# Kernel tuning notes

Measured on AMD Instinct MI355X. Metric: run time of the kernel, lower is better.

The kernel has to match this reference:

```python
import jax, jax.numpy as jnp
import numpy as np

# pywt db8 reconstruction low-pass filter (rec_lo); other filters derived per pywt conventions
_REC_LO = np.array([
    0.05441584224308161, 0.3128715909144659, 0.6756307362980128,
    0.5853546836548691, -0.015829105256023893, -0.2840155429624281,
    0.00047248457399797254, 0.128747426620186, -0.01736930100202211,
    -0.04408825393106472, 0.013981027917015516, 0.008746094047015655,
    -0.00487035299301066, -0.0003917403729959771, 0.0006754494059985568,
    -0.00011747678400228192], dtype=np.float64)
_F = 16
_REC_HI = np.array([(-1.0) ** k * _REC_LO[_F - 1 - k] for k in range(_F)])  # qmf
_DEC_LO = _REC_LO[::-1].copy()
_DEC_HI = _REC_HI[::-1].copy()
# lax.conv does cross-correlation; np.convolve flips the filter, so pre-flip here
_DEC_K = np.ascontiguousarray(np.stack([_DEC_LO[::-1], _DEC_HI[::-1]])[:, None, :])  # [2,1,F]
_REC_K = np.ascontiguousarray(np.stack([_REC_LO[::-1], _REC_HI[::-1]])[None, :, :])  # [1,2,F]
_THRESHOLD_FACTOR = 1.0


def _dwt_last(x):
    # single-level DWT along last axis, pywt 'symmetric' boundary mode
    shp = x.shape
    xf = x.reshape(-1, 1, shp[-1])
    xe = jnp.pad(xf, ((0, 0), (0, 0), (_F - 1, _F - 1)), mode='symmetric')[:, :, 1:]
    y = jax.lax.conv_general_dilated(xe, jnp.asarray(_DEC_K, x.dtype), (2,), 'VALID',
                                     dimension_numbers=('NCW', 'OIW', 'NCW'))  # [M,2,n]
    n = y.shape[-1]  # n = floor((N + F - 1) / 2)
    return y[:, 0].reshape(shp[:-1] + (n,)), y[:, 1].reshape(shp[:-1] + (n,))


def _idwt_last(ca, cd, out_len):
    # single-level inverse DWT along last axis; out_len = 2*n - F + 2
    shp = ca.shape
    n = shp[-1]
    m = int(np.prod(shp[:-1]))
    u = jnp.zeros((m, 2, 2 * n), ca.dtype)
    u = u.at[:, 0, ::2].set(ca.reshape(m, n)).at[:, 1, ::2].set(cd.reshape(m, n))
    ue = jnp.pad(u, ((0, 0), (0, 0), (_F - 1, _F - 1)))
    y = jax.lax.conv_general_dilated(ue, jnp.asarray(_REC_K, ca.dtype), (1,), 'VALID',
                                     dimension_numbers=('NCW', 'OIW', 'NCW'))[:, 0]
    return y[:, _F - 2:_F - 2 + out_len].reshape(shp[:-1] + (out_len,))


def _forward(x):
    B, H, W, C = x.shape
    M = B * C
    xm = jnp.transpose(x, (0, 3, 1, 2)).reshape(M, H, W)
    # level-1 wavedec2: rows (W axis) then columns (H axis)
    lo, hi = _dwt_last(xm)                               # [M,H,nW]
    ll, lh = _dwt_last(jnp.swapaxes(lo, -1, -2))         # [M,nW,nH]
    hl, hh = _dwt_last(jnp.swapaxes(hi, -1, -2))         # [M,nW,nH]
    # universal threshold from median abs of all detail subbands, per sample/channel
    det = jnp.concatenate([lh.reshape(M, -1), hl.reshape(M, -1), hh.reshape(M, -1)], axis=-1)
    sigma = jnp.median(jnp.abs(det), axis=-1) / 0.6745
    t = (sigma * jnp.sqrt(2.0 * jnp.log(float(H * W))) * _THRESHOLD_FACTOR)[:, None, None]
    soft = lambda c: jnp.sign(c) * jnp.maximum(jnp.abs(c) - t, 0.0)
    lh, hl, hh = soft(lh), soft(hl), soft(hh)
    # waverec2: inverse along H then along W
    nH = ll.shape[-1]
    Hr = 2 * nH - _F + 2
    rl = jnp.swapaxes(_idwt_last(ll, lh, Hr), -1, -2)    # [M,Hr,nW]
    rh = jnp.swapaxes(_idwt_last(hl, hh, Hr), -1, -2)    # [M,Hr,nW]
    nW = rl.shape[-1]
    y = _idwt_last(rl, rh, 2 * nW - _F + 2)              # [M,Hr,Wr]
    y = y[:, :H, :W].reshape(B, C, H, W)
    return jnp.transpose(y, (0, 2, 3, 1)).astype(x.dtype)


def setup_inputs() -> dict:
    key = jax.random.key(0)
    x = jax.random.normal(key, (32, 512, 512, 3), dtype=jnp.float32)
    return {"x": x}


def reference(x):
    return _forward(x)
```

## Files before the change

kernel.cpp:

```cpp
#include <hip/hip_runtime.h>
#include <math.h>

#define B_   32
#define H_   512
#define W_   512
#define C_   3
#define M_   96
#define NW_  263
#define NH_  263
#define DETPER 69169
#define DETTOT 207507
#define DETSTRIDE 207508
#define NVEC 51876
#define KRANK  103753u

#define SXS 144
#define CR  12

__device__ __constant__ float RLO[16] = {
    0.05441584224308161f,  0.3128715909144659f,   0.6756307362980128f,
    0.5853546836548691f,  -0.015829105256023893f, -0.2840155429624281f,
    0.00047248457399797254f, 0.128747426620186f,  -0.01736930100202211f,
   -0.04408825393106472f,  0.013981027917015516f,  0.008746094047015655f,
   -0.00487035299301066f, -0.0003917403729959771f, 0.0006754494059985568f,
   -0.00011747678400228192f};
__device__ __constant__ float RHI[16] = {
   -0.00011747678400228192f, -0.0006754494059985568f, -0.0003917403729959771f,
    0.00487035299301066f,     0.008746094047015655f,  -0.013981027917015516f,
   -0.04408825393106472f,     0.01736930100202211f,    0.128747426620186f,
   -0.00047248457399797254f, -0.2840155429624281f,     0.015829105256023893f,
    0.5853546836548691f,     -0.6756307362980128f,     0.3128715909144659f,
   -0.05441584224308161f};

__device__ __forceinline__ int refl(int q, int N) {
    if (q < 0)  return -q - 1;
    if (q >= N) return 2 * N - 1 - q;
    return q;
}

__device__ __forceinline__ float softthr(float v, float thr) {
    float a = fabsf(v) - thr;
    return a > 0.f ? copysignf(a, v) : 0.f;
}

__global__ __launch_bounds__(256) void k_zero(unsigned* __restrict__ p, int n) {
    int i = blockIdx.x * 256 + threadIdx.x;
    if (i < n) p[i] = 0u;
}

__global__ __launch_bounds__(256) void k_fwd(const float* __restrict__ x,
                                             float* __restrict__ ll,
                                             float* __restrict__ det) {
    __shared__ float sX[CR * SXS];
    __shared__ float sLO[46 * 64], sHI[46 * 64];
    const int m   = blockIdx.x;
    const int jw0 = blockIdx.y * 64;
    const int jh0 = blockIdx.z * 16;
    const int b = m / 3, c = m - 3 * (m / 3);
    const int tid = threadIdx.x;
    const int prow0 = 2 * jh0 - 14, pcol0 = 2 * jw0 - 14;
    for (int r0 = 0; r0 < 46; r0 += CR) {
        const int nr = (46 - r0) < CR ? (46 - r0) : CR;
        for (int l = tid; l < nr * 142; l += 256) {
            int rr = l / 142, cl = l - rr * 142;
            int h = refl(prow0 + r0 + rr, H_);
            int w = refl(pcol0 + cl, W_);
            sX[rr * SXS + cl] = x[((size_t)(b * H_ + h) * W_ + w) * C_ + c];
        }
        __syncthreads();
        for (int l = tid; l < nr * 64; l += 256) {
            int rr = l >> 6, j = l & 63;
            const float* px = &sX[rr * SXS + 2 * j];
            float al = 0.f, ah = 0.f;
#pragma unroll
            for (int k = 0; k < 16; ++k) {
                al = fmaf(px[k], RLO[k], al);
                ah = fmaf(px[k], RHI[k], ah);
            }
            sLO[(r0 + rr) * 64 + j] = al;
            sHI[(r0 + rr) * 64 + j] = ah;
        }
        __syncthreads();
    }
    const int tx = tid & 63, tg = tid >> 6;
    const int jw = jw0 + tx;
    if (jw >= NW_) return;
    float vl[22], vh[22];
#pragma unroll
    for (int s = 0; s < 22; ++s) {
        int row = 8 * tg + s;
        vl[s] = sLO[row * 64 + tx];
        vh[s] = sHI[row * 64 + tx];
    }
    float* llp = ll + (size_t)m * DETPER;
    float* dp  = det + (size_t)m * DETSTRIDE;
#pragma unroll
    for (int d = 0; d < 4; ++d) {
        int jh = jh0 + 4 * tg + d;
        if (jh >= NH_) continue;
        float a0 = 0.f, a1 = 0.f, a2 = 0.f, a3 = 0.f;
#pragma unroll
        for (int k = 0; k < 16; ++k) {
            float fl = vl[2 * d + k], fh = vh[2 * d + k];
            a0 = fmaf(fl, RLO[k], a0);
            a1 = fmaf(fl, RHI[k], a1);
            a2 = fmaf(fh, RLO[k], a2);
            a3 = fmaf(fh, RHI[k], a3);
        }
        size_t o = (size_t)jh * NW_ + jw;
        llp[o] = a0;
        dp[o] = a1;
        dp[DETPER + o] = a2;
        dp[2 * DETPER + o] = a3;
    }
}

__global__ __launch_bounds__(256) void k_hist1(const float* __restrict__ det,
                                               unsigned* __restrict__ hist) {
    __shared__ unsigned h[2048];
    const int tid = threadIdx.x, m = blockIdx.x;
    for (int i = tid; i < 2048; i += 256) h[i] = 0u;
    __syncthreads();
    const float* dp = det + (size_t)m * DETSTRIDE;
    const float4* dp4 = (const float4*)dp;
    const int stride = gridDim.y * 256;
    for (int v = blockIdx.y * 256 + tid; v < NVEC; v += stride) {
        float4 f = dp4[v];
        atomicAdd(&h[__float_as_uint(fabsf(f.x)) >> 21], 1u);
        atomicAdd(&h[__float_as_uint(fabsf(f.y)) >> 21], 1u);
        atomicAdd(&h[__float_as_uint(fabsf(f.z)) >> 21], 1u);
        atomicAdd(&h[__float_as_uint(fabsf(f.w)) >> 21], 1u);
    }
    if (blockIdx.y == 0 && tid < DETTOT - 4 * NVEC) {
        unsigned u = __float_as_uint(fabsf(dp[4 * NVEC + tid]));
        atomicAdd(&h[u >> 21], 1u);
    }
    __syncthreads();
    for (int i = tid; i < 2048; i += 256)
        if (h[i]) atomicAdd(&hist[m * 2048 + i], h[i]);
}

__global__ __launch_bounds__(256) void k_hist2(const float* __restrict__ det,
                                               const int* __restrict__ selBin1,
                                               unsigned* __restrict__ hist) {
    __shared__ unsigned h[2048];
    const int tid = threadIdx.x, m = blockIdx.x;
    const unsigned target = (unsigned)selBin1[m];
    for (int i = tid; i < 2048; i += 256) h[i] = 0u;
    __syncthreads();
    const float* dp = det + (size_t)m * DETSTRIDE;
    const float4* dp4 = (const float4*)dp;
    const int stride = gridDim.y * 256;
    for (int v = blockIdx.y * 256 + tid; v < NVEC; v += stride) {
        float4 f = dp4[v];
        unsigned a = __float_as_uint(fabsf(f.x));
        unsigned b = __float_as_uint(fabsf(f.y));
        unsigned c = __float_as_uint(fabsf(f.z));
        unsigned d = __float_as_uint(fabsf(f.w));
        if ((a >> 21) == target) atomicAdd(&h[(a >> 10) & 0x7FFu], 1u);
        if ((b >> 21) == target) atomicAdd(&h[(b >> 10) & 0x7FFu], 1u);
        if ((c >> 21) == target) atomicAdd(&h[(c >> 10) & 0x7FFu], 1u);
        if ((d >> 21) == target) atomicAdd(&h[(d >> 10) & 0x7FFu], 1u);
    }
    if (blockIdx.y == 0 && tid < DETTOT - 4 * NVEC) {
        unsigned u = __float_as_uint(fabsf(dp[4 * NVEC + tid]));
        if ((u >> 21) == target) atomicAdd(&h[(u >> 10) & 0x7FFu], 1u);
    }
    __syncthreads();
    for (int i = tid; i < 2048; i += 256)
        if (h[i]) atomicAdd(&hist[m * 2048 + i], h[i]);
}

__global__ __launch_bounds__(256) void k_hist3(const float* __restrict__ det,
                                               const int* __restrict__ selBin1,
                                               const int* __restrict__ selBin2,
                                               unsigned* __restrict__ hist) {
    __shared__ unsigned h[1024];
    const int tid = threadIdx.x, m = blockIdx.x;
    const unsigned target = ((unsigned)selBin1[m] << 11) | (unsigned)selBin2[m];
    for (int i = tid; i < 1024; i += 256) h[i] = 0u;
    __syncthreads();
    const float* dp = det + (size_t)m * DETSTRIDE;
    const float4* dp4 = (const float4*)dp;
    const int stride = gridDim.y * 256;
    for (int v = blockIdx.y * 256 + tid; v < NVEC; v += stride) {
        float4 f = dp4[v];
        unsigned a = __float_as_uint(fabsf(f.x));
        unsigned b = __float_as_uint(fabsf(f.y));
        unsigned c = __float_as_uint(fabsf(f.z));
        unsigned d = __float_as_uint(fabsf(f.w));
        if ((a >> 10) == target) atomicAdd(&h[a & 0x3FFu], 1u);
        if ((b >> 10) == target) atomicAdd(&h[b & 0x3FFu], 1u);
        if ((c >> 10) == target) atomicAdd(&h[c & 0x3FFu], 1u);
        if ((d >> 10) == target) atomicAdd(&h[d & 0x3FFu], 1u);
    }
    if (blockIdx.y == 0 && tid < DETTOT - 4 * NVEC) {
        unsigned u = __float_as_uint(fabsf(dp[4 * NVEC + tid]));
        if ((u >> 10) == target) atomicAdd(&h[u & 0x3FFu], 1u);
    }
    __syncthreads();
    for (int i = tid; i < 1024; i += 256)
        if (h[i]) atomicAdd(&hist[m * 1024 + i], h[i]);
}

__device__ int histSelect(unsigned* hist, int nb, unsigned rank, unsigned* rem) {
    __shared__ unsigned ps[256];
    __shared__ int s_bin;
    __shared__ unsigned s_rem;
    const int tid = threadIdx.x;
    if (tid == 0) { s_bin = 0; s_rem = 0; }
    const int per = nb >> 8;
    unsigned s = 0;
    for (int i = 0; i < per; ++i) s += hist[tid * per + i];
    ps[tid] = s;
    __syncthreads();
    for (int off = 1; off < 256; off <<= 1) {
        unsigned v = ps[tid];
        unsigned add = (tid >= off) ? ps[tid - off] : 0u;
        __syncthreads();
        ps[tid] = v + add;
        __syncthreads();
    }
    unsigned incl = ps[tid], excl = incl - s;
    if (rank >= excl && rank < incl) {
        unsigned cum = excl;
        for (int i = 0; i < per; ++i) {
            unsigned c = hist[tid * per + i];
            if (cum + c > rank) { s_bin = tid * per + i; s_rem = rank - cum; break; }
            cum += c;
        }
    }
    __syncthreads();
    int rbin = s_bin;
    unsigned rr = s_rem;
    __syncthreads();
    *rem = rr;
    return rbin;
}

__global__ __launch_bounds__(256) void k_sel2048(const unsigned* __restrict__ hist,
                                                 const unsigned* __restrict__ rankIn,
                                                 int* __restrict__ selBin,
                                                 unsigned* __restrict__ rankOut) {
    __shared__ unsigned h[2048];
    const int m = blockIdx.x, tid = threadIdx.x;
    for (int i = tid; i < 2048; i += 256) h[i] = hist[m * 2048 + i];
    __syncthreads();
    unsigned rank = rankIn ? rankIn[m] : KRANK;
    unsigned rem;
    int bin = histSelect(h, 2048, rank, &rem);
    if (tid == 0) { selBin[m] = bin; rankOut[m] = rem; }
}

__global__ __launch_bounds__(256) void k_sel3(const unsigned* __restrict__ hist,
                                              const unsigned* __restrict__ rankIn,
                                              const int* __restrict__ selBin1,
                                              const int* __restrict__ selBin2,
                                              float* __restrict__ tval) {
    __shared__ unsigned h[1024];
    const int m = blockIdx.x, tid = threadIdx.x;
    for (int i = tid; i < 1024; i += 256) h[i] = hist[m * 1024 + i];
    __syncthreads();
    unsigned rem;
    int low = histSelect(h, 1024, rankIn[m], &rem);
    if (tid == 0) {
        unsigned bits = ((unsigned)selBin1[m] << 21) | ((unsigned)selBin2[m] << 10) | (unsigned)low;
        double med = (double)__uint_as_float(bits);
        tval[m] = (float)(med / 0.6745 * 4.995327667046959);
    }
}

__global__ __launch_bounds__(256) void k_inv(const float* __restrict__ ll,
                                             const float* __restrict__ det,
                                             const float* __restrict__ tval,
                                             float* __restrict__ out) {
    __shared__ float sLL[23 * 40], sLH[23 * 40], sHL[23 * 40], sHH[23 * 40];
    __shared__ float sRL[32 * 40], sRH[32 * 40];
    const int m  = blockIdx.x;
    const int w0 = blockIdx.y * 64;
    const int t0 = blockIdx.z * 32;
    const int b = m / 3, c = m - 3 * (m / 3);
    const int tid = threadIdx.x;
    const float thr = tval[m];
    const int jW0 = w0 >> 1, s0 = t0 >> 1;
    const float* llp = ll + (size_t)m * DETPER;
    const float* dp  = det + (size_t)m * DETSTRIDE;
    for (int l = tid; l < 23 * 39; l += 256) {
        int rr = l / 39, cc = l - rr * 39;
        size_t o = (size_t)(s0 + rr) * NW_ + (jW0 + cc);
        int li = rr * 40 + cc;
        sLL[li] = llp[o];
        sLH[li] = softthr(dp[o], thr);
        sHL[li] = softthr(dp[DETPER + o], thr);
        sHH[li] = softthr(dp[2 * DETPER + o], thr);
    }
    __syncthreads();
    for (int l = tid; l < 32 * 39; l += 256) {
        int tr = l / 39, cc = l - tr * 39;
        int srow = tr >> 1, r = tr & 1;
        float aL = 0.f, aH = 0.f;
#pragma unroll
        for (int a = 0; a < 8; ++a) {
            int li = (srow + 7 - a) * 40 + cc;
            float wl = RLO[2 * a + r], wh = RHI[2 * a + r];
            aL = fmaf(sLL[li], wl, fmaf(sLH[li], wh, aL));
            aH = fmaf(sHL[li], wl, fmaf(sHH[li], wh, aH));
        }
        sRL[tr * 40 + cc] = aL;
        sRH[tr * 40 + cc] = aH;
    }
    __syncthreads();
    for (int l = tid; l < 32 * 64; l += 256) {
        int tr = l >> 6, wloc = l & 63;
        int r = wloc & 1, jb = (wloc >> 1) + 7;
        float acc = 0.f;
#pragma unroll
        for (int a = 0; a < 8; ++a) {
            int li = tr * 40 + jb - a;
            acc = fmaf(sRL[li], RLO[2 * a + r], fmaf(sRH[li], RHI[2 * a + r], acc));
        }
        out[((size_t)(b * H_ + (t0 + tr)) * W_ + (w0 + wloc)) * C_ + c] = acc;
    }
}

extern "C" void kernel_launch(void* const* d_in, const int* in_sizes, int n_in,
                              void* d_out, int out_size, void* d_ws, size_t ws_size,
                              hipStream_t stream) {
    const float* x = (const float*)d_in[0];
    float* out = (float*)d_out;

    char* ws = (char*)d_ws;
    float* ll  = (float*)ws; ws += (size_t)M_ * DETPER * 4;
    float* det = (float*)ws; ws += (size_t)M_ * DETSTRIDE * 4;
    unsigned* hist1 = (unsigned*)ws; ws += (size_t)M_ * 2048 * 4;
    unsigned* hist2 = (unsigned*)ws; ws += (size_t)M_ * 2048 * 4;
    unsigned* hist3 = (unsigned*)ws; ws += (size_t)M_ * 1024 * 4;
    int*      selBin1 = (int*)ws;      ws += M_ * 4;
    int*      selBin2 = (int*)ws;      ws += M_ * 4;
    unsigned* rank1   = (unsigned*)ws; ws += M_ * 4;
    unsigned* rank2   = (unsigned*)ws; ws += M_ * 4;
    float*    tval    = (float*)ws;    ws += M_ * 4;

    const int histWords = M_ * (2048 + 2048 + 1024);
    k_zero   <<<dim3((histWords + 255) / 256), 256, 0, stream>>>(hist1, histWords);
    k_fwd    <<<dim3(M_, 5, 17),  256, 0, stream>>>(x, ll, det);
    k_hist1  <<<dim3(M_, 16),     256, 0, stream>>>(det, hist1);
    k_sel2048<<<dim3(M_),         256, 0, stream>>>(hist1, nullptr, selBin1, rank1);
    k_hist2  <<<dim3(M_, 16),     256, 0, stream>>>(det, selBin1, hist2);
    k_sel2048<<<dim3(M_),         256, 0, stream>>>(hist2, rank1, selBin2, rank2);
    k_hist3  <<<dim3(M_, 16),     256, 0, stream>>>(det, selBin1, selBin2, hist3);
    k_sel3   <<<dim3(M_),         256, 0, stream>>>(hist3, rank2, selBin1, selBin2, tval);
    k_inv    <<<dim3(M_, 8, 16),  256, 0, stream>>>(ll, det, tval, out);
}
```

Baseline: 435.7 us.

## Fuse first histogram pass into forward DWT and compact candidates for third pass

The top-level 11-bit histogram of detail magnitudes is now built in shared memory inside the forward DWT kernel, so the separate first histogram pass over the detail buffer is dropped. The second histogram pass also writes the values that fall in the selected bin to a per-sample candidate list. The third pass then scans only that short list instead of the full detail array. This saves two full reads of roughly 80 MB, at the cost of extra shared memory and atomics in the forward kernel, plus a fallback path when the list overflows or the workspace is too small.

```diff
diff --git a/kernel.cpp b/kernel.cpp
--- a/kernel.cpp
+++ b/kernel.cpp
@@ -16,6 +16,9 @@
 
 #define SXS 144
 #define CR  12
+
+#define CAP  32768
+#define LCAP 4096
 
 __device__ __constant__ float RLO[16] = {
     0.05441584224308161f,  0.3128715909144659f,   0.6756307362980128f,
@@ -50,15 +53,18 @@
 
 __global__ __launch_bounds__(256) void k_fwd(const float* __restrict__ x,
                                              float* __restrict__ ll,
-                                             float* __restrict__ det) {
+                                             float* __restrict__ det,
+                                             unsigned* __restrict__ hist) {
     __shared__ float sX[CR * SXS];
     __shared__ float sLO[46 * 64], sHI[46 * 64];
+    __shared__ unsigned hh[2048];
     const int m   = blockIdx.x;
     const int jw0 = blockIdx.y * 64;
     const int jh0 = blockIdx.z * 16;
     const int b = m / 3, c = m - 3 * (m / 3);
     const int tid = threadIdx.x;
     const int prow0 = 2 * jh0 - 14, pcol0 = 2 * jw0 - 14;
+    for (int i = tid; i < 2048; i += 256) hh[i] = 0u;
     for (int r0 = 0; r0 < 46; r0 += CR) {
         const int nr = (46 - r0) < CR ? (46 - r0) : CR;
         for (int l = tid; l < nr * 142; l += 256) {
@@ -84,7 +90,7 @@
     }
     const int tx = tid & 63, tg = tid >> 6;
     const int jw = jw0 + tx;
-    if (jw >= NW_) return;
+    const bool vw = (jw < NW_);
     float vl[22], vh[22];
 #pragma unroll
     for (int s = 0; s < 22; ++s) {
@@ -97,7 +103,6 @@
 #pragma unroll
     for (int d = 0; d < 4; ++d) {
         int jh = jh0 + 4 * tg + d;
-        if (jh >= NH_) continue;
         float a0 = 0.f, a1 = 0.f, a2 = 0.f, a3 = 0.f;
 #pragma unroll
         for (int k = 0; k < 16; ++k) {
@@ -107,66 +112,72 @@
             a2 = fmaf(fh, RLO[k], a2);
             a3 = fmaf(fh, RHI[k], a3);
         }
-        size_t o = (size_t)jh * NW_ + jw;
-        llp[o] = a0;
-        dp[o] = a1;
-        dp[DETPER + o] = a2;
-        dp[2 * DETPER + o] = a3;
-    }
-}
-
-__global__ __launch_bounds__(256) void k_hist1(const float* __restrict__ det,
-                                               unsigned* __restrict__ hist) {
+        if (vw && jh < NH_) {
+            size_t o = (size_t)jh * NW_ + jw;
+            llp[o] = a0;
+            dp[o] = a1;
+            dp[DETPER + o] = a2;
+            dp[2 * DETPER + o] = a3;
+            atomicAdd(&hh[__float_as_uint(fabsf(a1)) >> 21], 1u);
+            atomicAdd(&hh[__float_as_uint(fabsf(a2)) >> 21], 1u);
+            atomicAdd(&hh[__float_as_uint(fabsf(a3)) >> 21], 1u);
+        }
+    }
+    __syncthreads();
+    for (int i = tid; i < 2048; i += 256)
+        if (hh[i]) atomicAdd(&hist[m * 2048 + i], hh[i]);
+}
+
+__global__ __launch_bounds__(256) void k_hist2(const float* __restrict__ det,
+                                               const int* __restrict__ selBin1,
+                                               unsigned* __restrict__ hist,
+                                               unsigned* __restrict__ cnt,
+                                               unsigned* __restrict__ list,
+                                               int docap) {
     __shared__ unsigned h[2048];
+    __shared__ unsigned cbuf[LCAP];
+    __shared__ unsigned ccnt, sbase;
     const int tid = threadIdx.x, m = blockIdx.x;
+    const unsigned target = (unsigned)selBin1[m];
     for (int i = tid; i < 2048; i += 256) h[i] = 0u;
+    if (tid == 0) ccnt = 0u;
     __syncthreads();
     const float* dp = det + (size_t)m * DETSTRIDE;
     const float4* dp4 = (const float4*)dp;
     const int stride = gridDim.y * 256;
+    unsigned* const lst = list + (size_t)m * CAP;
+    auto take = [&](unsigned u) {
+        if ((u >> 21) == target) {
+            atomicAdd(&h[(u >> 10) & 0x7FFu], 1u);
+            if (docap) {
+                unsigned p = atomicAdd(&ccnt, 1u);
+                if (p < LCAP) cbuf[p] = u;
+                else {
+                    unsigned g = atomicAdd(&cnt[m], 1u);
+                    if (g < CAP) lst[g] = u;
+                }
+            }
+        }
+    };
     for (int v = blockIdx.y * 256 + tid; v < NVEC; v += stride) {
         float4 f = dp4[v];
-        atomicAdd(&h[__float_as_uint(fabsf(f.x)) >> 21], 1u);
-        atomicAdd(&h[__float_as_uint(fabsf(f.y)) >> 21], 1u);
-        atomicAdd(&h[__float_as_uint(fabsf(f.z)) >> 21], 1u);
-        atomicAdd(&h[__float_as_uint(fabsf(f.w)) >> 21], 1u);
-    }
-    if (blockIdx.y == 0 && tid < DETTOT - 4 * NVEC) {
-        unsigned u = __float_as_uint(fabsf(dp[4 * NVEC + tid]));
-        atomicAdd(&h[u >> 21], 1u);
-    }
-    __syncthreads();
-    for (int i = tid; i < 2048; i += 256)
-        if (h[i]) atomicAdd(&hist[m * 2048 + i], h[i]);
-}
-
-__global__ __launch_bounds__(256) void k_hist2(const float* __restrict__ det,
-                                               const int* __restrict__ selBin1,
-                                               unsigned* __restrict__ hist) {
-    __shared__ unsigned h[2048];
-    const int tid = threadIdx.x, m = blockIdx.x;
-    const unsigned target = (unsigned)selBin1[m];
-    for (int i = tid; i < 2048; i += 256) h[i] = 0u;
-    __syncthreads();
-    const float* dp = det + (size_t)m * DETSTRIDE;
-    const float4* dp4 = (const float4*)dp;
-    const int stride = gridDim.y * 256;
-    for (int v = blockIdx.y * 256 + tid; v < NVEC; v += stride) {
-        float4 f = dp4[v];
-        unsigned a = __float_as_uint(fabsf(f.x));
-        unsigned b = __float_as_uint(fabsf(f.y));
-        unsigned c = __float_as_uint(fabsf(f.z));
-        unsigned d = __float_as_uint(fabsf(f.w));
-        if ((a >> 21) == target) atomicAdd(&h[(a >> 10) & 0x7FFu], 1u);
-        if ((b >> 21) == target) atomicAdd(&h[(b >> 10) & 0x7FFu], 1u);
-        if ((c >> 21) == target) atomicAdd(&h[(c >> 10) & 0x7FFu], 1u);
-        if ((d >> 21) == target) atomicAdd(&h[(d >> 10) & 0x7FFu], 1u);
-    }
-    if (blockIdx.y == 0 && tid < DETTOT - 4 * NVEC) {
-        unsigned u = __float_as_uint(fabsf(dp[4 * NVEC + tid]));
-        if ((u >> 21) == target) atomicAdd(&h[(u >> 10) & 0x7FFu], 1u);
-    }
-    __syncthreads();
+        take(__float_as_uint(fabsf(f.x)));
+        take(__float_as_uint(fabsf(f.y)));
+        take(__float_as_uint(fabsf(f.z)));
+        take(__float_as_uint(fabsf(f.w)));
+    }
+    if (blockIdx.y == 0 && tid < DETTOT - 4 * NVEC)
+        take(__float_as_uint(fabsf(dp[4 * NVEC + tid])));
+    __syncthreads();
+    if (docap) {
+        unsigned n = ccnt < LCAP ? ccnt : LCAP;
+        if (tid == 0) sbase = atomicAdd(&cnt[m], n);
+        __syncthreads();
+        for (unsigned i = tid; i < n; i += 256) {
+            unsigned p = sbase + i;
+            if (p < CAP) lst[p] = cbuf[i];
+        }
+    }
     for (int i = tid; i < 2048; i += 256)
         if (h[i]) atomicAdd(&hist[m * 2048 + i], h[i]);
 }
@@ -174,29 +185,44 @@
 __global__ __launch_bounds__(256) void k_hist3(const float* __restrict__ det,
                                                const int* __restrict__ selBin1,
                                                const int* __restrict__ selBin2,
+                                               const unsigned* __restrict__ cnt,
+                                               const unsigned* __restrict__ list,
+                                               int docap,
                                                unsigned* __restrict__ hist) {
     __shared__ unsigned h[1024];
     const int tid = threadIdx.x, m = blockIdx.x;
-    const unsigned target = ((unsigned)selBin1[m] << 11) | (unsigned)selBin2[m];
     for (int i = tid; i < 1024; i += 256) h[i] = 0u;
     __syncthreads();
-    const float* dp = det + (size_t)m * DETSTRIDE;
-    const float4* dp4 = (const float4*)dp;
-    const int stride = gridDim.y * 256;
-    for (int v = blockIdx.y * 256 + tid; v < NVEC; v += stride) {
-        float4 f = dp4[v];
-        unsigned a = __float_as_uint(fabsf(f.x));
-        unsigned b = __float_as_uint(fabsf(f.y));
-        unsigned c = __float_as_uint(fabsf(f.z));
-        unsigned d = __float_as_uint(fabsf(f.w));
-        if ((a >> 10) == target) atomicAdd(&h[a & 0x3FFu], 1u);
-        if ((b >> 10) == target) atomicAdd(&h[b & 0x3FFu], 1u);
-        if ((c >> 10) == target) atomicAdd(&h[c & 0x3FFu], 1u);
-        if ((d >> 10) == target) atomicAdd(&h[d & 0x3FFu], 1u);
-    }
-    if (blockIdx.y == 0 && tid < DETTOT - 4 * NVEC) {
-        unsigned u = __float_as_uint(fabsf(dp[4 * NVEC + tid]));
-        if ((u >> 10) == target) atomicAdd(&h[u & 0x3FFu], 1u);
+    const unsigned n = cnt[m];
+    const bool fast = docap && (n <= CAP);
+    if (fast) {
+        const unsigned b2 = (unsigned)selBin2[m];
+        const unsigned* lst = list + (size_t)m * CAP;
+        const int stride = gridDim.y * 256;
+        for (unsigned i = blockIdx.y * 256 + tid; i < n; i += stride) {
+            unsigned u = lst[i];
+            if (((u >> 10) & 0x7FFu) == b2) atomicAdd(&h[u & 0x3FFu], 1u);
+        }
+    } else {
+        const unsigned target = ((unsigned)selBin1[m] << 11) | (unsigned)selBin2[m];
+        const float* dp = det + (size_t)m * DETSTRIDE;
+        const float4* dp4 = (const float4*)dp;
+        const int stride = gridDim.y * 256;
+        for (int v = blockIdx.y * 256 + tid; v < NVEC; v += stride) {
+            float4 f = dp4[v];
+            unsigned a = __float_as_uint(fabsf(f.x));
+            unsigned b = __float_as_uint(fabsf(f.y));
+            unsigned c = __float_as_uint(fabsf(f.z));
+            unsigned d = __float_as_uint(fabsf(f.w));
+            if ((a >> 10) == target) atomicAdd(&h[a & 0x3FFu], 1u);
+            if ((b >> 10) == target) atomicAdd(&h[b & 0x3FFu], 1u);
+            if ((c >> 10) == target) atomicAdd(&h[c & 0x3FFu], 1u);
+            if ((d >> 10) == target) atomicAdd(&h[d & 0x3FFu], 1u);
+        }
+        if (blockIdx.y == 0 && tid < DETTOT - 4 * NVEC) {
+            unsigned u = __float_as_uint(fabsf(dp[4 * NVEC + tid]));
+            if ((u >> 10) == target) atomicAdd(&h[u & 0x3FFu], 1u);
+        }
     }
     __syncthreads();
     for (int i = tid; i < 1024; i += 256)
@@ -335,20 +361,22 @@
     unsigned* hist1 = (unsigned*)ws; ws += (size_t)M_ * 2048 * 4;
     unsigned* hist2 = (unsigned*)ws; ws += (size_t)M_ * 2048 * 4;
     unsigned* hist3 = (unsigned*)ws; ws += (size_t)M_ * 1024 * 4;
+    unsigned* cnt   = (unsigned*)ws;   ws += M_ * 4;
     int*      selBin1 = (int*)ws;      ws += M_ * 4;
     int*      selBin2 = (int*)ws;      ws += M_ * 4;
     unsigned* rank1   = (unsigned*)ws; ws += M_ * 4;
     unsigned* rank2   = (unsigned*)ws; ws += M_ * 4;
     float*    tval    = (float*)ws;    ws += M_ * 4;
-
-    const int histWords = M_ * (2048 + 2048 + 1024);
+    unsigned* list    = (unsigned*)ws; ws += (size_t)M_ * CAP * 4;
+    const int docap = (ws_size >= (size_t)((char*)(list + (size_t)M_ * CAP) - (char*)d_ws)) ? 1 : 0;
+
+    const int histWords = M_ * (2048 + 2048 + 1024) + M_;
     k_zero   <<<dim3((histWords + 255) / 256), 256, 0, stream>>>(hist1, histWords);
-    k_fwd    <<<dim3(M_, 5, 17),  256, 0, stream>>>(x, ll, det);
-    k_hist1  <<<dim3(M_, 16),     256, 0, stream>>>(det, hist1);
+    k_fwd    <<<dim3(M_, 5, 17),  256, 0, stream>>>(x, ll, det, hist1);
     k_sel2048<<<dim3(M_),         256, 0, stream>>>(hist1, nullptr, selBin1, rank1);
-    k_hist2  <<<dim3(M_, 16),     256, 0, stream>>>(det, selBin1, hist2);
+    k_hist2  <<<dim3(M_, 16),     256, 0, stream>>>(det, selBin1, hist2, cnt, list, docap);
     k_sel2048<<<dim3(M_),         256, 0, stream>>>(hist2, rank1, selBin2, rank2);
-    k_hist3  <<<dim3(M_, 16),     256, 0, stream>>>(det, selBin1, selBin2, hist3);
+    k_hist3  <<<dim3(M_, 16),     256, 0, stream>>>(det, selBin1, selBin2, cnt, list, docap, hist3);
     k_sel3   <<<dim3(M_),         256, 0, stream>>>(hist3, rank2, selBin1, selBin2, tval);
     k_inv    <<<dim3(M_, 8, 16),  256, 0, stream>>>(ll, det, tval, out);
 }
```

Result: slower. 449.4 us (+3.1%).

## Remap block indices for XCD locality and register-tile inverse DWT passes

Applied to the files above, without the earlier changes.

Block indices of the forward and inverse kernels are linearised and remapped so that consecutive blocks dispatched to the same XCD (lin & 7) work on contiguous tiles of the same batch image. The goal is better L2 reuse of overlapping halos and of the interleaved channels. The inverse kernel's two shared-memory passes are also rewritten: the column pass has each thread compute 4 columns by 2 output rows using float4 LDS loads. The row pass has each thread load 12 intermediate values into registers and produce 8 outputs, cutting LDS traffic and index arithmetic. This relies on the exact grid dimensions and leaves most threads idle in the first pass (160 of 256).

```diff
diff --git a/kernel.cpp b/kernel.cpp
--- a/kernel.cpp
+++ b/kernel.cpp
@@ -53,10 +53,14 @@
                                              float* __restrict__ det) {
     __shared__ float sX[CR * SXS];
     __shared__ float sLO[46 * 64], sHI[46 * 64];
-    const int m   = blockIdx.x;
-    const int jw0 = blockIdx.y * 64;
-    const int jh0 = blockIdx.z * 16;
-    const int b = m / 3, c = m - 3 * (m / 3);
+    const int lin = blockIdx.x + 96 * blockIdx.y + 480 * blockIdx.z;
+    const int xcd = lin & 7, t = lin >> 3;
+    const int c = t % 3, ul = t / 3;
+    const int u = xcd * 340 + ul;
+    const int b = u / 85, r = u - 85 * b;
+    const int jw0 = (r % 5) * 64;
+    const int jh0 = (r / 5) * 16;
+    const int m = 3 * b + c;
     const int tid = threadIdx.x;
     const int prow0 = 2 * jh0 - 14, pcol0 = 2 * jw0 - 14;
     for (int r0 = 0; r0 < 46; r0 += CR) {
@@ -276,10 +280,14 @@
                                              float* __restrict__ out) {
     __shared__ float sLL[23 * 40], sLH[23 * 40], sHL[23 * 40], sHH[23 * 40];
     __shared__ float sRL[32 * 40], sRH[32 * 40];
-    const int m  = blockIdx.x;
-    const int w0 = blockIdx.y * 64;
-    const int t0 = blockIdx.z * 32;
-    const int b = m / 3, c = m - 3 * (m / 3);
+    const int lin = blockIdx.x + 96 * blockIdx.y + 768 * blockIdx.z;
+    const int xcd = lin & 7, t = lin >> 3;
+    const int c = t % 3, ul = t / 3;
+    const int u = xcd * 512 + ul;
+    const int b = u >> 7, r = u & 127;
+    const int w0 = (r & 7) * 64;
+    const int t0 = (r >> 3) * 32;
+    const int m = 3 * b + c;
     const int tid = threadIdx.x;
     const float thr = tval[m];
     const int jW0 = w0 >> 1, s0 = t0 >> 1;
@@ -295,31 +303,63 @@
         sHH[li] = softthr(dp[2 * DETPER + o], thr);
     }
     __syncthreads();
-    for (int l = tid; l < 32 * 39; l += 256) {
-        int tr = l / 39, cc = l - tr * 39;
-        int srow = tr >> 1, r = tr & 1;
-        float aL = 0.f, aH = 0.f;
+    for (int l = tid; l < 160; l += 256) {
+        int s = l / 10, q = l - 10 * (l / 10);
+        float4 aL0 = make_float4(0.f, 0.f, 0.f, 0.f), aL1 = aL0, aH0 = aL0, aH1 = aL0;
 #pragma unroll
         for (int a = 0; a < 8; ++a) {
-            int li = (srow + 7 - a) * 40 + cc;
-            float wl = RLO[2 * a + r], wh = RHI[2 * a + r];
-            aL = fmaf(sLL[li], wl, fmaf(sLH[li], wh, aL));
-            aH = fmaf(sHL[li], wl, fmaf(sHH[li], wh, aH));
-        }
-        sRL[tr * 40 + cc] = aL;
-        sRH[tr * 40 + cc] = aH;
-    }
-    __syncthreads();
-    for (int l = tid; l < 32 * 64; l += 256) {
-        int tr = l >> 6, wloc = l & 63;
-        int r = wloc & 1, jb = (wloc >> 1) + 7;
-        float acc = 0.f;
-#pragma unroll
-        for (int a = 0; a < 8; ++a) {
-            int li = tr * 40 + jb - a;
-            acc = fmaf(sRL[li], RLO[2 * a + r], fmaf(sRH[li], RHI[2 * a + r], acc));
-        }
-        out[((size_t)(b * H_ + (t0 + tr)) * W_ + (w0 + wloc)) * C_ + c] = acc;
+            int li = (s + 7 - a) * 40 + 4 * q;
+            float4 vLL = *(const float4*)&sLL[li];
+            float4 vLH = *(const float4*)&sLH[li];
+            float4 vHL = *(const float4*)&sHL[li];
+            float4 vHH = *(const float4*)&sHH[li];
+            float w00 = RLO[2 * a],     h00 = RHI[2 * a];
+            float w01 = RLO[2 * a + 1], h01 = RHI[2 * a + 1];
+            aL0.x = fmaf(vLL.x, w00, fmaf(vLH.x, h00, aL0.x));
+            aL0.y = fmaf(vLL.y, w00, fmaf(vLH.y, h00, aL0.y));
+            aL0.z = fmaf(vLL.z, w00, fmaf(vLH.z, h00, aL0.z));
+            aL0.w = fmaf(vLL.w, w00, fmaf(vLH.w, h00, aL0.w));
+            aL1.x = fmaf(vLL.x, w01, fmaf(vLH.x, h01, aL1.x));
+            aL1.y = fmaf(vLL.y, w01, fmaf(vLH.y, h01, aL1.y));
+            aL1.z = fmaf(vLL.z, w01, fmaf(vLH.z, h01, aL1.z));
+            aL1.w = fmaf(vLL.w, w01, fmaf(vLH.w, h01, aL1.w));
+            aH0.x = fmaf(vHL.x, w00, fmaf(vHH.x, h00, aH0.x));
+            aH0.y = fmaf(vHL.y, w00, fmaf(vHH.y, h00, aH0.y));
+            aH0.z = fmaf(vHL.z, w00, fmaf(vHH.z, h00, aH0.z));
+            aH0.w = fmaf(vHL.w, w00, fmaf(vHH.w, h00, aH0.w));
+            aH1.x = fmaf(vHL.x, w01, fmaf(vHH.x, h01, aH1.x));
+            aH1.y = fmaf(vHL.y, w01, fmaf(vHH.y, h01, aH1.y));
+            aH1.z = fmaf(vHL.z, w01, fmaf(vHH.z, h01, aH1.z));
+            aH1.w = fmaf(vHL.w, w01, fmaf(vHH.w, h01, aH1.w));
+        }
+        *(float4*)&sRL[(2 * s) * 40 + 4 * q]     = aL0;
+        *(float4*)&sRL[(2 * s + 1) * 40 + 4 * q] = aL1;
+        *(float4*)&sRH[(2 * s) * 40 + 4 * q]     = aH0;
+        *(float4*)&sRH[(2 * s + 1) * 40 + 4 * q] = aH1;
+    }
+    __syncthreads();
+    {
+        const int tr = tid >> 3, jg = tid & 7;
+        const float4* pl = (const float4*)&sRL[tr * 40 + 4 * jg];
+        const float4* ph = (const float4*)&sRH[tr * 40 + 4 * jg];
+        float4 L0 = pl[0], L1 = pl[1], L2 = pl[2];
+        float4 K0 = ph[0], K1 = ph[1], K2 = ph[2];
+        float rl[12] = {L0.x,L0.y,L0.z,L0.w, L1.x,L1.y,L1.z,L1.w, L2.x,L2.y,L2.z,L2.w};
+        float rh[12] = {K0.x,K0.y,K0.z,K0.w, K1.x,K1.y,K1.z,K1.w, K2.x,K2.y,K2.z,K2.w};
+        size_t obase = ((size_t)(b * H_ + (t0 + tr)) * W_ + (w0 + 8 * jg)) * C_ + c;
+#pragma unroll
+        for (int u2 = 0; u2 < 4; ++u2) {
+#pragma unroll
+            for (int rp = 0; rp < 2; ++rp) {
+                float acc = 0.f;
+#pragma unroll
+                for (int a = 0; a < 8; ++a) {
+                    int sdx = u2 + 7 - a;
+                    acc = fmaf(rl[sdx], RLO[2 * a + rp], fmaf(rh[sdx], RHI[2 * a + rp], acc));
+                }
+                out[obase + (size_t)(2 * u2 + rp) * C_] = acc;
+            }
+        }
     }
 }
 
```

Result: slower. 462.7 us (+6.2%).
